# Kernel optimization log

Hardware: AMD Instinct MI355X
Metric: run time of the kernel (lower is better)

## Reference

```python
import jax, jax.numpy as jnp
import numpy as np

N, D, H1, K = 4096, 128, 256, 128


def setup_inputs() -> dict:
    key = jax.random.key(0)
    ks = jax.random.split(key, 8)
    A = jax.random.uniform(ks[3], (D, D), dtype=jnp.float32)
    A = A * (1.0 - jnp.eye(D, dtype=jnp.float32))  # DAG prob mask, no self-loops
    return {
        "x": jax.random.normal(ks[0], (N, D), dtype=jnp.float32),
        "weight": jax.random.normal(ks[1], (D, D), dtype=jnp.float32) * 0.1,
        "bias": jax.random.normal(ks[2], (1, D), dtype=jnp.float32) * 0.1,
        "A": A,
        "W1": jax.random.normal(ks[4], (D, H1), dtype=jnp.float32) * 0.1,
        "b1": jax.random.normal(ks[5], (H1,), dtype=jnp.float32) * 0.1,
        "W2": jax.random.normal(ks[6], (H1, K), dtype=jnp.float32) * 0.1,
        "b2": jax.random.normal(ks[7], (K,), dtype=jnp.float32) * 0.1,
    }


def reference(x, weight, bias, A, W1, b1, W2, b2):
    # to_adj (eval path): masked weights
    W = weight * A                                   # [D, D]
    y = x @ W + bias                                 # [N, D]
    # __expand__ builds diag(y[n]) [N,D,D]; since e[n,i,:] = y[n,i]*I[i,:],
    # the first Linear collapses to a per-row scaling of W1 (same math, fused):
    # e @ W1 -> y[n,i] * W1[i,:]
    h1 = jax.nn.relu(y[:, :, None] * W1[None, :, :] + b1)   # [N, D, H1]
    f = (h1 @ W2 + b2).sum(axis=2)                   # [N, D] (sum over output dim)
    # h_func, method='gnn'
    I = jnp.eye(D, dtype=x.dtype)
    A2 = jnp.square(W)
    M = I + A2 / D
    E = jnp.linalg.matrix_power(M, D - 1)
    h_val = (E.T * M).sum() - D
    # l1_reg (same prob mask in eval)
    reg = jnp.abs(W).sum()
    return (f, h_val, reg)
```

## Files before the change

kernel.cpp:

```cpp
#include <hip/hip_runtime.h>

#define NN 4096
#define DD 128
#define HH1 256

#define WS_S    0
#define WS_S2   16384
#define WS_S3   32768
#define WS_S4   49152
#define WS_W    65536
#define WS_W2S  81920
#define WS_PAIR 82176
#define WS_B2S  82688
#define WS_TACC 82696
#define WS_DONE 82708
#define WS_REGP 82712
#define WS_XT   82944
#define WS_REQ_FLOATS 607232
#define WS_REQ_BYTES  (WS_REQ_FLOATS * 4UL)

#define O_S    0
#define O_S2   16384
#define O_S3   32768
#define O_S4   49152
#define O_W2S  65536
#define O_B2S  65792
#define O_TACC 65808
#define O_DONE 65824
#define O_REGP 65840

__device__ __forceinline__ float waveReduce(float v) {
#pragma unroll
  for (int off = 32; off > 0; off >>= 1) v += __shfl_down(v, off, 64);
  return v;
}


__global__ __launch_bounds__(256) void kA2(
    const float* __restrict__ weight, const float* __restrict__ Amat,
    const float* __restrict__ W2, const float* __restrict__ b2,
    const float* __restrict__ b1v, const float* __restrict__ x,
    float* __restrict__ ws) {
  const int b = blockIdx.x, tid = threadIdx.x;
  __shared__ float s_lds[DD * DD];
  __shared__ float xs[128 * 133];
  if (b < 64) {
    const float4* w4 = (const float4*)weight;
    const float4* a4 = (const float4*)Amat;
    float4* s4 = (float4*)s_lds;
    const float inv = 1.0f / 128.0f;
    for (int e = tid; e < DD * DD / 4; e += 256) {
      float4 wv = w4[e], av = a4[e], o;
      float t;
      t = wv.x * av.x; o.x = t * t * inv;
      t = wv.y * av.y; o.y = t * t * inv;
      t = wv.z * av.z; o.z = t * t * inv;
      t = wv.w * av.w; o.w = t * t * inv;
      s4[e] = o;
    }
    __syncthreads();
    const int i = (b << 1) + (tid >> 7), j = tid & 127;
    const float* row = &s_lds[i * DD];
    float acc = 0.f;
#pragma unroll 8
    for (int k = 0; k < DD; ++k) acc = fmaf(row[k], s_lds[k * DD + j], acc);
    ws[WS_S2 + i * DD + j] = acc;
  } else if (b < 72) {
    const int base = (b - 64) * 2048;
    const float inv = 1.0f / 128.0f;
    for (int e = tid; e < 2048; e += 256) {
      const int idx = base + e;
      const float w = weight[idx] * Amat[idx];
      ws[WS_W + idx] = w;
      ws[WS_S + idx] = w * w * inv;
    }
  } else if (b == 72) {
    const float4* r = (const float4*)(W2 + tid * 128);
    float4 s4 = make_float4(0.f, 0.f, 0.f, 0.f);
#pragma unroll 8
    for (int k = 0; k < 32; ++k) {
      const float4 v = r[k];
      s4.x += v.x; s4.y += v.y; s4.z += v.z; s4.w += v.w;
    }
    const float w2sv = (s4.x + s4.y) + (s4.z + s4.w);
    ws[WS_W2S + tid] = w2sv;
    ((float2*)(ws + WS_PAIR))[tid] = make_float2(b1v[tid], w2sv);
  } else if (b == 73) {
    __shared__ float red[4];
    float v = (tid < 128) ? b2[tid] : 0.f;
    v = waveReduce(v);
    if ((tid & 63) == 0) red[tid >> 6] = v;
    __syncthreads();
    if (tid == 0) ws[WS_B2S] = (red[0] + red[1]) + (red[2] + red[3]);
    if (tid >= 64 && tid < 74) ws[WS_TACC + (tid - 64)] = 0.f;
    if (tid == 96) *(unsigned int*)(ws + WS_DONE) = 0u;
  } else if (b < 82) {
    const int bb = b - 74;
    const int base = bb * 2048;
    float s = 0.f;
    for (int e = tid; e < 2048; e += 256) {
      const int idx = base + e;
      s += fabsf(weight[idx] * Amat[idx]);
    }
    s = waveReduce(s);
    __shared__ float red2[4];
    if ((tid & 63) == 0) red2[tid >> 6] = s;
    __syncthreads();
    if (tid == 0) ws[WS_REGP + bb] = (red2[0] + red2[1]) + (red2[2] + red2[3]);
  } else {
    const int n0 = (b - 82) * 128;
    const float4* x4 = (const float4*)x;
    for (int e = tid; e < 4096; e += 256) {
      const int r = e >> 5, c = e & 31;
      const float4 v = x4[(n0 + r) * 32 + c];
      float* p = &xs[r * 133 + (c << 2)];
      p[0] = v.x; p[1] = v.y; p[2] = v.z; p[3] = v.w;
    }
    __syncthreads();
    float* xT = ws + WS_XT;
    const int c = tid & 31, ks = tid >> 5;
#pragma unroll 4
    for (int m = 0; m < 16; ++m) {
      const int k = ks + (m << 3);
      float4 o;
      o.x = xs[((c << 2) + 0) * 133 + k];
      o.y = xs[((c << 2) + 1) * 133 + k];
      o.z = xs[((c << 2) + 2) * 133 + k];
      o.w = xs[((c << 2) + 3) * 133 + k];
      *(float4*)&xT[k * NN + n0 + (c << 2)] = o;
    }
  }
}

__global__ __launch_bounds__(256) void kS34(float* __restrict__ ws) {
  const int tid = threadIdx.x;
  const int sb = blockIdx.x;
  const bool isS4 = sb >= 64;
  const int mb = isS4 ? sb - 64 : sb;
  const float* __restrict__ L = ws + WS_S2;
  const float* __restrict__ R = ws + (isS4 ? WS_S2 : WS_S);
  float* __restrict__ O = ws + (isS4 ? WS_S4 : WS_S3);
  const int i = (mb << 1) + (tid >> 7), j = tid & 127;
  float acc = 0.f;
#pragma unroll 8
  for (int k = 0; k < DD; ++k) acc = fmaf(L[i * DD + k], R[k * DD + j], acc);
  O[i * DD + j] = acc;
}

__global__ __launch_bounds__(256) void kC4(const float* __restrict__ W1,
                                           const float* __restrict__ bias,
                                           float* __restrict__ ws,
                                           float* __restrict__ out) {
  const int tid = threadIdx.x;
  if (blockIdx.x < 512) {
    __shared__ float ts[256 * 5];
    const int fb = blockIdx.x;
    const int n0 = (fb >> 5) << 8, i0 = (fb & 31) << 2;
    const int w = tid >> 6, l = tid & 63;
    const int iu = __builtin_amdgcn_readfirstlane(i0 + w);
    const float* __restrict__ xT = ws + WS_XT;
    const float* __restrict__ Wm = ws + WS_W;

    float t[4] = {0.f, 0.f, 0.f, 0.f};
#pragma unroll 8
    for (int k = 0; k < DD; ++k) {
      const float wv = Wm[k * DD + iu];
      const float4 xv = *(const float4*)&xT[k * NN + n0 + (l << 2)];
      t[0] = fmaf(xv.x, wv, t[0]);
      t[1] = fmaf(xv.y, wv, t[1]);
      t[2] = fmaf(xv.z, wv, t[2]);
      t[3] = fmaf(xv.w, wv, t[3]);
    }
    const float bv = bias[iu];
#pragma unroll
    for (int q = 0; q < 4; ++q) t[q] += bv;

    const float sb2 = ws[WS_B2S];
    float acc[4];
#pragma unroll
    for (int q = 0; q < 4; ++q) acc[q] = sb2;
    const float* __restrict__ W1row = W1 + iu * HH1;
    const float2* __restrict__ pr = (const float2*)(ws + WS_PAIR);
#pragma unroll 8
    for (int j = 0; j < HH1; ++j) {
      const float sw1 = W1row[j];
      const float2 p = pr[j];
      const float vb = p.x;
#pragma unroll
      for (int q = 0; q < 4; ++q) {
        const float h = fmaxf(fmaf(t[q], sw1, vb), 0.f);
        acc[q] = fmaf(h, p.y, acc[q]);
      }
    }
#pragma unroll
    for (int q = 0; q < 4; ++q) ts[((l << 2) + q) * 5 + w] = acc[q];
    __syncthreads();
    const int m = tid;
    float4 o;
    o.x = ts[m * 5 + 0]; o.y = ts[m * 5 + 1];
    o.z = ts[m * 5 + 2]; o.w = ts[m * 5 + 3];
    *(float4*)&out[(n0 + m) * DD + i0] = o;
    return;
  }
  const int tb = blockIdx.x - 512;
  const int i = (tb << 1) + (tid >> 7), j = tid & 127;
  const float* S1 = ws + WS_S;
  const float* S2 = ws + WS_S2;
  const float* S3 = ws + WS_S3;
  const float* S4 = ws + WS_S4;
  const float a1 = S1[i * DD + j], a2 = S2[i * DD + j], a3 = S3[i * DD + j];
  const float b1t = S1[j * DD + i], b2t = S2[j * DD + i],
              b3t = S3[j * DD + i], b4t = S4[j * DD + i];
  float e7 = 0.f;
#pragma unroll 8
  for (int k = 0; k < DD; ++k) e7 = fmaf(S3[i * DD + k], S4[k * DD + j], e7);
  float c[10];
  c[0] = a1 * b1t; c[1] = a2 * b1t; c[2] = a2 * b2t; c[3] = a3 * b2t;
  c[4] = a3 * b3t; c[5] = a3 * b4t; c[6] = e7 * b1t; c[7] = e7 * b2t;
  c[8] = e7 * b3t; c[9] = e7 * b4t;
  __shared__ float red[4][10];
#pragma unroll
  for (int m = 0; m < 10; ++m) {
    const float v = waveReduce(c[m]);
    if ((tid & 63) == 0) red[tid >> 6][m] = v;
  }
  __syncthreads();
  if (tid == 0) {
    float* tacc = ws + WS_TACC;
    for (int m = 0; m < 10; ++m)
      atomicAdd(&tacc[m], (red[0][m] + red[1][m]) + (red[2][m] + red[3][m]));
    __threadfence();
    unsigned int* done = (unsigned int*)(ws + WS_DONE);
    const unsigned int old = atomicAdd(done, 1u);
    if (old == 63u) {
      __threadfence();
      double h = 0.0, C = 8128.0;
      for (int kk = 2; kk <= 11; ++kk) {
        const float tv = atomicAdd(&tacc[kk - 2], 0.0f);
        h += C * (double)tv;
        C = C * (double)(128 - kk) / (double)(kk + 1);
      }
      float reg = 0.f;
      for (int m = 0; m < 8; ++m) reg += ws[WS_REGP + m];
      out[NN * DD] = (float)h;
      out[NN * DD + 1] = reg;
    }
  }
}

__global__ __launch_bounds__(256) void kA_old(
    const float* __restrict__ weight, const float* __restrict__ Amat,
    const float* __restrict__ W2, const float* __restrict__ b2,
    float* __restrict__ ws) {
  const int b = blockIdx.x, tid = threadIdx.x;
  if (b < 64) {
    __shared__ float s_lds[DD * DD];
    const float4* w4 = (const float4*)weight;
    const float4* a4 = (const float4*)Amat;
    float4* s4 = (float4*)s_lds;
    const float inv = 1.0f / 128.0f;
    for (int e = tid; e < DD * DD / 4; e += 256) {
      float4 wv = w4[e], av = a4[e], o;
      float t;
      t = wv.x * av.x; o.x = t * t * inv;
      t = wv.y * av.y; o.y = t * t * inv;
      t = wv.z * av.z; o.z = t * t * inv;
      t = wv.w * av.w; o.w = t * t * inv;
      s4[e] = o;
    }
    __syncthreads();
    const int i = (b << 1) + (tid >> 7), j = tid & 127;
    const float* row = &s_lds[i * DD];
    float acc = 0.f;
#pragma unroll 8
    for (int k = 0; k < DD; ++k) acc = fmaf(row[k], s_lds[k * DD + j], acc);
    ws[O_S2 + i * DD + j] = acc;
  } else if (b < 72) {
    const int base = (b - 64) * 2048;
    const float inv = 1.0f / 128.0f;
    for (int e = tid; e < 2048; e += 256) {
      const int idx = base + e;
      const float w = weight[idx] * Amat[idx];
      ws[O_S + idx] = w * w * inv;
    }
  } else if (b == 72) {
    const float4* r = (const float4*)(W2 + tid * 128);
    float4 s4 = make_float4(0.f, 0.f, 0.f, 0.f);
#pragma unroll 8
    for (int k = 0; k < 32; ++k) {
      const float4 v = r[k];
      s4.x += v.x; s4.y += v.y; s4.z += v.z; s4.w += v.w;
    }
    ws[O_W2S + tid] = (s4.x + s4.y) + (s4.z + s4.w);
  } else if (b == 73) {
    __shared__ float red[4];
    float v = (tid < 128) ? b2[tid] : 0.f;
    v = waveReduce(v);
    if ((tid & 63) == 0) red[tid >> 6] = v;
    __syncthreads();
    if (tid == 0) ws[O_B2S] = (red[0] + red[1]) + (red[2] + red[3]);
    if (tid >= 64 && tid < 74) ws[O_TACC + (tid - 64)] = 0.f;
    if (tid == 96) *(unsigned int*)(ws + O_DONE) = 0u;
  } else {
    const int bb = b - 74;
    const int base = bb * 2048;
    float s = 0.f;
    for (int e = tid; e < 2048; e += 256) {
      const int idx = base + e;
      s += fabsf(weight[idx] * Amat[idx]);
    }
    s = waveReduce(s);
    __shared__ float red[4];
    if ((tid & 63) == 0) red[tid >> 6] = s;
    __syncthreads();
    if (tid == 0) ws[O_REGP + bb] = (red[0] + red[1]) + (red[2] + red[3]);
  }
}

__global__ __launch_bounds__(256) void kB_old(
    const float* __restrict__ x, const float* __restrict__ weight,
    const float* __restrict__ Amat, const float* __restrict__ bias,
    const float* __restrict__ W1, const float* __restrict__ b1v,
    float* __restrict__ ws, float* __restrict__ out) {
  const int tid = threadIdx.x;
  if (blockIdx.x < 128) {
    const int sb = blockIdx.x;
    const bool isS4 = sb >= 64;
    const int mb = isS4 ? sb - 64 : sb;
    const float* __restrict__ L = ws + O_S2;
    const float* __restrict__ R = ws + (isS4 ? O_S2 : O_S);
    float* __restrict__ O = ws + (isS4 ? O_S4 : O_S3);
    const int i = (mb << 1) + (tid >> 7), j = tid & 127;
    float acc = 0.f;
#pragma unroll 8
    for (int k = 0; k < DD; ++k) acc = fmaf(L[i * DD + k], R[k * DD + j], acc);
    O[i * DD + j] = acc;
    return;
  }
  __shared__ float xs[64 * 132];
  __shared__ float4 fq[4 * 256];
  __shared__ float wcol[4 * 128];
  __shared__ float ts[64 * 5];
  const int fb = blockIdx.x - 128;
  const int i0 = (fb & 31) << 2, n0 = (fb >> 5) << 6;
  const float4* x4 = (const float4*)x;
  for (int e = tid; e < 64 * 32; e += 256) {
    const int r = e >> 5, c = e & 31;
    *(float4*)&xs[r * 132 + (c << 2)] = x4[(n0 + r) * 32 + c];
  }
  for (int e = tid; e < 512; e += 256) {
    const int w = e >> 7, k = e & 127;
    const int gi = k * DD + i0 + w;
    wcol[(w << 7) + k] = weight[gi] * Amat[gi];
  }
  const float* w2s = ws + O_W2S;
  for (int e = tid; e < 1024; e += 256) {
    const int w = e >> 8, j = e & 255;
    fq[(w << 8) + j] = make_float4(W1[(i0 + w) * HH1 + j], b1v[j], w2s[j], 0.f);
  }
  __syncthreads();
  const int w = tid >> 6, l = tid & 63;
  float t = bias[i0 + w];
  const float4* xr = (const float4*)&xs[l * 132];
  const float4* wc = (const float4*)&wcol[w << 7];
#pragma unroll
  for (int k = 0; k < 32; ++k) {
    const float4 xv = xr[k], wv = wc[k];
    t = fmaf(xv.x, wv.x, t);
    t = fmaf(xv.y, wv.y, t);
    t = fmaf(xv.z, wv.z, t);
    t = fmaf(xv.w, wv.w, t);
  }
  float acc = ws[O_B2S];
  const float4* fp = &fq[w << 8];
#pragma unroll 8
  for (int j = 0; j < HH1; ++j) {
    const float4 c = fp[j];
    acc = fmaf(fmaxf(fmaf(t, c.x, c.y), 0.f), c.z, acc);
  }
  ts[l * 5 + w] = acc;
  __syncthreads();
  if (tid < 64) {
    const float4 o = make_float4(ts[tid * 5 + 0], ts[tid * 5 + 1],
                                 ts[tid * 5 + 2], ts[tid * 5 + 3]);
    *(float4*)&out[(n0 + tid) * DD + i0] = o;
  }
}

__global__ __launch_bounds__(256) void kC_old(float* __restrict__ ws,
                                              float* __restrict__ out) {
  const int tid = threadIdx.x;
  const int i = (blockIdx.x << 1) + (tid >> 7), j = tid & 127;
  const float* S1 = ws + O_S;
  const float* S2 = ws + O_S2;
  const float* S3 = ws + O_S3;
  const float* S4 = ws + O_S4;
  const float a1 = S1[i * DD + j], a2 = S2[i * DD + j], a3 = S3[i * DD + j];
  const float b1t = S1[j * DD + i], b2t = S2[j * DD + i],
              b3t = S3[j * DD + i], b4t = S4[j * DD + i];
  float e7 = 0.f;
#pragma unroll 8
  for (int k = 0; k < DD; ++k) e7 = fmaf(S3[i * DD + k], S4[k * DD + j], e7);
  float c[10];
  c[0] = a1 * b1t; c[1] = a2 * b1t; c[2] = a2 * b2t; c[3] = a3 * b2t;
  c[4] = a3 * b3t; c[5] = a3 * b4t; c[6] = e7 * b1t; c[7] = e7 * b2t;
  c[8] = e7 * b3t; c[9] = e7 * b4t;
  __shared__ float red[4][10];
#pragma unroll
  for (int m = 0; m < 10; ++m) {
    const float v = waveReduce(c[m]);
    if ((tid & 63) == 0) red[tid >> 6][m] = v;
  }
  __syncthreads();
  if (tid == 0) {
    float* tacc = ws + O_TACC;
    for (int m = 0; m < 10; ++m)
      atomicAdd(&tacc[m], (red[0][m] + red[1][m]) + (red[2][m] + red[3][m]));
    __threadfence();
    unsigned int* done = (unsigned int*)(ws + O_DONE);
    const unsigned int old = atomicAdd(done, 1u);
    if (old == 63u) {
      __threadfence();
      double h = 0.0, C = 8128.0;
      for (int kk = 2; kk <= 11; ++kk) {
        const float tv = atomicAdd(&tacc[kk - 2], 0.0f);
        h += C * (double)tv;
        C = C * (double)(128 - kk) / (double)(kk + 1);
      }
      float reg = 0.f;
      for (int m = 0; m < 8; ++m) reg += ws[O_REGP + m];
      out[NN * DD] = (float)h;
      out[NN * DD + 1] = reg;
    }
  }
}

extern "C" void kernel_launch(void* const* d_in, const int* in_sizes, int n_in,
                              void* d_out, int out_size, void* d_ws,
                              size_t ws_size, hipStream_t stream) {
  const float* x      = (const float*)d_in[0];
  const float* weight = (const float*)d_in[1];
  const float* bias   = (const float*)d_in[2];
  const float* Amat   = (const float*)d_in[3];
  const float* W1     = (const float*)d_in[4];
  const float* b1v    = (const float*)d_in[5];
  const float* W2     = (const float*)d_in[6];
  const float* b2     = (const float*)d_in[7];
  float* out = (float*)d_out;
  float* ws  = (float*)d_ws;

  if (ws_size >= WS_REQ_BYTES) {
    kA2<<<114, 256, 0, stream>>>(weight, Amat, W2, b2, b1v, x, ws);
    kS34<<<128, 256, 0, stream>>>(ws);
    kC4<<<576, 256, 0, stream>>>(W1, bias, ws, out);
  } else {
    kA_old<<<82, 256, 0, stream>>>(weight, Amat, W2, b2, ws);
    kB_old<<<128 + 2048, 256, 0, stream>>>(x, weight, Amat, bias, W1, b1v, ws,
                                           out);
    kC_old<<<64, 256, 0, stream>>>(ws, out);
  }
}
```

Before: 125.8 us.

## Halve rows per thread in fused MLP kernel and add transposed masked weight

The main f-computation kernel now gives each thread 2 rows instead of 4, which doubles the block count to 1024. The x-transpose blocks are also halved in size, so kA2 launches more blocks. A transposed copy of the masked weight W is written so each wave reads its row of W contiguously instead of with a strided column access. The aim is more parallelism and better latency hiding on the ALU-bound 256-wide hidden loop. The cost is more per-block overhead, less reuse of W1 and pair loads per thread, and half the threads sitting idle during the output store.

```diff
diff --git a/kernel.cpp b/kernel.cpp
--- a/kernel.cpp
+++ b/kernel.cpp
@@ -15,8 +15,9 @@
 #define WS_TACC 82696
 #define WS_DONE 82708
 #define WS_REGP 82712
-#define WS_XT   82944
-#define WS_REQ_FLOATS 607232
+#define WS_WT   82944
+#define WS_XT   99328
+#define WS_REQ_FLOATS 623616
 #define WS_REQ_BYTES  (WS_REQ_FLOATS * 4UL)
 
 #define O_S    0
@@ -43,7 +44,7 @@
     float* __restrict__ ws) {
   const int b = blockIdx.x, tid = threadIdx.x;
   __shared__ float s_lds[DD * DD];
-  __shared__ float xs[128 * 133];
+  __shared__ float xs[64 * 133];
   if (b < 64) {
     const float4* w4 = (const float4*)weight;
     const float4* a4 = (const float4*)Amat;
@@ -71,7 +72,9 @@
     for (int e = tid; e < 2048; e += 256) {
       const int idx = base + e;
       const float w = weight[idx] * Amat[idx];
+      const int k = idx >> 7, i = idx & 127;
       ws[WS_W + idx] = w;
+      ws[WS_WT + i * DD + k] = w;
       ws[WS_S + idx] = w * w * inv;
     }
   } else if (b == 72) {
@@ -108,9 +111,9 @@
     __syncthreads();
     if (tid == 0) ws[WS_REGP + bb] = (red2[0] + red2[1]) + (red2[2] + red2[3]);
   } else {
-    const int n0 = (b - 82) * 128;
+    const int n0 = (b - 82) * 64;
     const float4* x4 = (const float4*)x;
-    for (int e = tid; e < 4096; e += 256) {
+    for (int e = tid; e < 2048; e += 256) {
       const int r = e >> 5, c = e & 31;
       const float4 v = x4[(n0 + r) * 32 + c];
       float* p = &xs[r * 133 + (c << 2)];
@@ -118,10 +121,10 @@
     }
     __syncthreads();
     float* xT = ws + WS_XT;
-    const int c = tid & 31, ks = tid >> 5;
-#pragma unroll 4
-    for (int m = 0; m < 16; ++m) {
-      const int k = ks + (m << 3);
+    const int c = tid & 15, ks = tid >> 4;
+#pragma unroll
+    for (int m = 0; m < 8; ++m) {
+      const int k = ks + (m << 4);
       float4 o;
       o.x = xs[((c << 2) + 0) * 133 + k];
       o.y = xs[((c << 2) + 1) * 133 + k];
@@ -147,62 +150,58 @@
   O[i * DD + j] = acc;
 }
 
-__global__ __launch_bounds__(256) void kC4(const float* __restrict__ W1,
+__global__ __launch_bounds__(256) void kC5(const float* __restrict__ W1,
                                            const float* __restrict__ bias,
                                            float* __restrict__ ws,
                                            float* __restrict__ out) {
   const int tid = threadIdx.x;
-  if (blockIdx.x < 512) {
-    __shared__ float ts[256 * 5];
+  if (blockIdx.x < 1024) {
+    __shared__ float ts[128 * 5];
     const int fb = blockIdx.x;
-    const int n0 = (fb >> 5) << 8, i0 = (fb & 31) << 2;
+    const int n0 = (fb >> 5) << 7, i0 = (fb & 31) << 2;
     const int w = tid >> 6, l = tid & 63;
     const int iu = __builtin_amdgcn_readfirstlane(i0 + w);
     const float* __restrict__ xT = ws + WS_XT;
-    const float* __restrict__ Wm = ws + WS_W;
-
-    float t[4] = {0.f, 0.f, 0.f, 0.f};
+    const float* __restrict__ wr = ws + WS_WT + iu * DD;
+
+    float t0 = 0.f, t1 = 0.f;
 #pragma unroll 8
     for (int k = 0; k < DD; ++k) {
-      const float wv = Wm[k * DD + iu];
-      const float4 xv = *(const float4*)&xT[k * NN + n0 + (l << 2)];
-      t[0] = fmaf(xv.x, wv, t[0]);
-      t[1] = fmaf(xv.y, wv, t[1]);
-      t[2] = fmaf(xv.z, wv, t[2]);
-      t[3] = fmaf(xv.w, wv, t[3]);
+      const float wv = wr[k];
+      const float2 xv = *(const float2*)&xT[k * NN + n0 + (l << 1)];
+      t0 = fmaf(xv.x, wv, t0);
+      t1 = fmaf(xv.y, wv, t1);
     }
     const float bv = bias[iu];
-#pragma unroll
-    for (int q = 0; q < 4; ++q) t[q] += bv;
+    t0 += bv;
+    t1 += bv;
 
     const float sb2 = ws[WS_B2S];
-    float acc[4];
-#pragma unroll
-    for (int q = 0; q < 4; ++q) acc[q] = sb2;
+    float a0 = sb2, a1 = sb2;
     const float* __restrict__ W1row = W1 + iu * HH1;
     const float2* __restrict__ pr = (const float2*)(ws + WS_PAIR);
 #pragma unroll 8
     for (int j = 0; j < HH1; ++j) {
       const float sw1 = W1row[j];
       const float2 p = pr[j];
-      const float vb = p.x;
-#pragma unroll
-      for (int q = 0; q < 4; ++q) {
-        const float h = fmaxf(fmaf(t[q], sw1, vb), 0.f);
-        acc[q] = fmaf(h, p.y, acc[q]);
-      }
-    }
-#pragma unroll
-    for (int q = 0; q < 4; ++q) ts[((l << 2) + q) * 5 + w] = acc[q];
-    __syncthreads();
-    const int m = tid;
-    float4 o;
-    o.x = ts[m * 5 + 0]; o.y = ts[m * 5 + 1];
-    o.z = ts[m * 5 + 2]; o.w = ts[m * 5 + 3];
-    *(float4*)&out[(n0 + m) * DD + i0] = o;
+      const float h0 = fmaxf(fmaf(t0, sw1, p.x), 0.f);
+      const float h1 = fmaxf(fmaf(t1, sw1, p.x), 0.f);
+      a0 = fmaf(h0, p.y, a0);
+      a1 = fmaf(h1, p.y, a1);
+    }
+    ts[((l << 1) + 0) * 5 + w] = a0;
+    ts[((l << 1) + 1) * 5 + w] = a1;
+    __syncthreads();
+    if (tid < 128) {
+      const int m = tid;
+      float4 o;
+      o.x = ts[m * 5 + 0]; o.y = ts[m * 5 + 1];
+      o.z = ts[m * 5 + 2]; o.w = ts[m * 5 + 3];
+      *(float4*)&out[(n0 + m) * DD + i0] = o;
+    }
     return;
   }
-  const int tb = blockIdx.x - 512;
+  const int tb = blockIdx.x - 1024;
   const int i = (tb << 1) + (tid >> 7), j = tid & 127;
   const float* S1 = ws + WS_S;
   const float* S2 = ws + WS_S2;
@@ -450,9 +449,9 @@
   float* ws  = (float*)d_ws;
 
   if (ws_size >= WS_REQ_BYTES) {
-    kA2<<<114, 256, 0, stream>>>(weight, Amat, W2, b2, b1v, x, ws);
+    kA2<<<146, 256, 0, stream>>>(weight, Amat, W2, b2, b1v, x, ws);
     kS34<<<128, 256, 0, stream>>>(ws);
-    kC4<<<576, 256, 0, stream>>>(W1, bias, ws, out);
+    kC5<<<1088, 256, 0, stream>>>(W1, bias, ws, out);
   } else {
     kA_old<<<82, 256, 0, stream>>>(weight, Amat, W2, b2, ws);
     kB_old<<<128 + 2048, 256, 0, stream>>>(x, weight, Amat, bias, W1, b1v, ws,
```

Measured after the change: 125.5 us. Within noise of the previous version (-0.3%).

## Replace per-row ReLU MLP loop with piecewise-linear breakpoint lookup

Applied to the files above, without the earlier changes.

For each input dimension i, the sum over H1 of relu(y*W1[i,j]+b1[j])*w2s[j] is a piecewise-linear function of y. A new kernel precomputes its sorted breakpoints and prefix-summed slope and intercept tables, using a bitonic sort and a scan. The main kernel then evaluates f with an 8-step binary search in LDS and one FMA, replacing the 256-iteration loop. It also stores a transposed masked weight so the y computation reads contiguously, and splits the x transpose into smaller blocks. The costs are an extra precompute pass, more workspace, and possible float reassociation differences.

```diff
diff --git a/kernel.cpp b/kernel.cpp
--- a/kernel.cpp
+++ b/kernel.cpp
@@ -15,8 +15,12 @@
 #define WS_TACC 82696
 #define WS_DONE 82708
 #define WS_REGP 82712
-#define WS_XT   82944
-#define WS_REQ_FLOATS 607232
+#define WS_WT   82944
+#define WS_XT   99328
+#define WS_TH   623616
+#define WS_A    656384
+#define WS_B    689280
+#define WS_REQ_FLOATS 722176
 #define WS_REQ_BYTES  (WS_REQ_FLOATS * 4UL)
 
 #define O_S    0
@@ -43,7 +47,7 @@
     float* __restrict__ ws) {
   const int b = blockIdx.x, tid = threadIdx.x;
   __shared__ float s_lds[DD * DD];
-  __shared__ float xs[128 * 133];
+  __shared__ float xs[64 * 133];
   if (b < 64) {
     const float4* w4 = (const float4*)weight;
     const float4* a4 = (const float4*)Amat;
@@ -71,7 +75,9 @@
     for (int e = tid; e < 2048; e += 256) {
       const int idx = base + e;
       const float w = weight[idx] * Amat[idx];
+      const int k = idx >> 7, i = idx & 127;
       ws[WS_W + idx] = w;
+      ws[WS_WT + i * DD + k] = w;
       ws[WS_S + idx] = w * w * inv;
     }
   } else if (b == 72) {
@@ -108,9 +114,9 @@
     __syncthreads();
     if (tid == 0) ws[WS_REGP + bb] = (red2[0] + red2[1]) + (red2[2] + red2[3]);
   } else {
-    const int n0 = (b - 82) * 128;
+    const int n0 = (b - 82) * 64;
     const float4* x4 = (const float4*)x;
-    for (int e = tid; e < 4096; e += 256) {
+    for (int e = tid; e < 2048; e += 256) {
       const int r = e >> 5, c = e & 31;
       const float4 v = x4[(n0 + r) * 32 + c];
       float* p = &xs[r * 133 + (c << 2)];
@@ -118,10 +124,10 @@
     }
     __syncthreads();
     float* xT = ws + WS_XT;
-    const int c = tid & 31, ks = tid >> 5;
-#pragma unroll 4
-    for (int m = 0; m < 16; ++m) {
-      const int k = ks + (m << 3);
+    const int c = tid & 15, ks = tid >> 4;
+#pragma unroll
+    for (int m = 0; m < 8; ++m) {
+      const int k = ks + (m << 4);
       float4 o;
       o.x = xs[((c << 2) + 0) * 133 + k];
       o.y = xs[((c << 2) + 1) * 133 + k];
@@ -132,39 +138,120 @@
   }
 }
 
-__global__ __launch_bounds__(256) void kS34(float* __restrict__ ws) {
+__global__ __launch_bounds__(256) void kPS(const float* __restrict__ W1,
+                                           const float* __restrict__ b1v,
+                                           float* __restrict__ ws) {
   const int tid = threadIdx.x;
-  const int sb = blockIdx.x;
-  const bool isS4 = sb >= 64;
-  const int mb = isS4 ? sb - 64 : sb;
-  const float* __restrict__ L = ws + WS_S2;
-  const float* __restrict__ R = ws + (isS4 ? WS_S2 : WS_S);
-  float* __restrict__ O = ws + (isS4 ? WS_S4 : WS_S3);
-  const int i = (mb << 1) + (tid >> 7), j = tid & 127;
-  float acc = 0.f;
-#pragma unroll 8
-  for (int k = 0; k < DD; ++k) acc = fmaf(L[i * DD + k], R[k * DD + j], acc);
-  O[i * DD + j] = acc;
-}
-
-__global__ __launch_bounds__(256) void kC4(const float* __restrict__ W1,
-                                           const float* __restrict__ bias,
+  if (blockIdx.x < 128) {
+    const int sb = blockIdx.x;
+    const bool isS4 = sb >= 64;
+    const int mb = isS4 ? sb - 64 : sb;
+    const float* __restrict__ L = ws + WS_S2;
+    const float* __restrict__ R = ws + (isS4 ? WS_S2 : WS_S);
+    float* __restrict__ O = ws + (isS4 ? WS_S4 : WS_S3);
+    const int i = (mb << 1) + (tid >> 7), j = tid & 127;
+    float acc = 0.f;
+#pragma unroll 8
+    for (int k = 0; k < DD; ++k) acc = fmaf(L[i * DD + k], R[k * DD + j], acc);
+    O[i * DD + j] = acc;
+    return;
+  }
+  const int i = blockIdx.x - 128;
+  __shared__ float kT[256], kS[256], kC[256];
+  __shared__ float redb[8];
+  __shared__ float base2[2];
+  const int j = tid;
+  const float w = W1[i * HH1 + j];
+  const float w2s = ws[WS_W2S + j];
+  const float bj = b1v[j];
+  const float s = w * w2s, c = bj * w2s;
+  float th, ds, dc, bs, bc;
+  if (w > 0.f) {
+    th = -bj / w; ds = s; dc = c; bs = 0.f; bc = 0.f;
+  } else if (w < 0.f) {
+    th = -bj / w; ds = -s; dc = -c; bs = s; bc = c;
+  } else {
+    th = 3.4e38f; ds = 0.f; dc = 0.f; bs = 0.f; bc = fmaxf(bj, 0.f) * w2s;
+  }
+  {
+    const float rs = waveReduce(bs), rc = waveReduce(bc);
+    if ((tid & 63) == 0) {
+      redb[tid >> 6] = rs;
+      redb[4 + (tid >> 6)] = rc;
+    }
+  }
+  kT[tid] = th; kS[tid] = ds; kC[tid] = dc;
+  __syncthreads();
+  if (tid == 0) {
+    base2[0] = (redb[0] + redb[1]) + (redb[2] + redb[3]);
+    base2[1] = (redb[4] + redb[5]) + (redb[6] + redb[7]);
+  }
+  for (int kk = 2; kk <= 256; kk <<= 1) {
+    for (int jj = kk >> 1; jj > 0; jj >>= 1) {
+      __syncthreads();
+      const int ixj = tid ^ jj;
+      if (ixj > tid) {
+        const bool up = ((tid & kk) == 0);
+        const float ta = kT[tid], tb = kT[ixj];
+        if ((ta > tb) == up) {
+          kT[tid] = tb; kT[ixj] = ta;
+          const float sa = kS[tid], sb = kS[ixj];
+          kS[tid] = sb; kS[ixj] = sa;
+          const float ca = kC[tid], cb = kC[ixj];
+          kC[tid] = cb; kC[ixj] = ca;
+        }
+      }
+    }
+  }
+  __syncthreads();
+  for (int off = 1; off < 256; off <<= 1) {
+    float vs = 0.f, vc = 0.f;
+    if (tid >= off) { vs = kS[tid - off]; vc = kC[tid - off]; }
+    __syncthreads();
+    kS[tid] += vs; kC[tid] += vc;
+    __syncthreads();
+  }
+  const float b_s = base2[0], b_c = base2[1];
+  ws[WS_TH + i * 256 + tid] = kT[tid];
+  ws[WS_A + i * 257 + tid + 1] = b_s + kS[tid];
+  ws[WS_B + i * 257 + tid + 1] = b_c + kC[tid];
+  if (tid == 0) {
+    ws[WS_A + i * 257] = b_s;
+    ws[WS_B + i * 257] = b_c;
+  }
+}
+
+__global__ __launch_bounds__(256) void kC6(const float* __restrict__ bias,
                                            float* __restrict__ ws,
                                            float* __restrict__ out) {
   const int tid = threadIdx.x;
   if (blockIdx.x < 512) {
+    __shared__ float lT[4 * 256];
+    __shared__ float lA[4 * 257];
+    __shared__ float lB[4 * 257];
     __shared__ float ts[256 * 5];
     const int fb = blockIdx.x;
     const int n0 = (fb >> 5) << 8, i0 = (fb & 31) << 2;
     const int w = tid >> 6, l = tid & 63;
     const int iu = __builtin_amdgcn_readfirstlane(i0 + w);
+
+#pragma unroll
+    for (int q = 0; q < 4; ++q) {
+      lT[(q << 8) + tid] = ws[WS_TH + (i0 + q) * 256 + tid];
+      lA[q * 257 + tid] = ws[WS_A + (i0 + q) * 257 + tid];
+      lB[q * 257 + tid] = ws[WS_B + (i0 + q) * 257 + tid];
+      if (tid == 0) {
+        lA[q * 257 + 256] = ws[WS_A + (i0 + q) * 257 + 256];
+        lB[q * 257 + 256] = ws[WS_B + (i0 + q) * 257 + 256];
+      }
+    }
+
     const float* __restrict__ xT = ws + WS_XT;
-    const float* __restrict__ Wm = ws + WS_W;
-
+    const float* __restrict__ wr = ws + WS_WT + iu * DD;
     float t[4] = {0.f, 0.f, 0.f, 0.f};
 #pragma unroll 8
     for (int k = 0; k < DD; ++k) {
-      const float wv = Wm[k * DD + iu];
+      const float wv = wr[k];
       const float4 xv = *(const float4*)&xT[k * NN + n0 + (l << 2)];
       t[0] = fmaf(xv.x, wv, t[0]);
       t[1] = fmaf(xv.y, wv, t[1]);
@@ -172,28 +259,23 @@
       t[3] = fmaf(xv.w, wv, t[3]);
     }
     const float bv = bias[iu];
-#pragma unroll
-    for (int q = 0; q < 4; ++q) t[q] += bv;
-
     const float sb2 = ws[WS_B2S];
-    float acc[4];
-#pragma unroll
-    for (int q = 0; q < 4; ++q) acc[q] = sb2;
-    const float* __restrict__ W1row = W1 + iu * HH1;
-    const float2* __restrict__ pr = (const float2*)(ws + WS_PAIR);
-#pragma unroll 8
-    for (int j = 0; j < HH1; ++j) {
-      const float sw1 = W1row[j];
-      const float2 p = pr[j];
-      const float vb = p.x;
-#pragma unroll
-      for (int q = 0; q < 4; ++q) {
-        const float h = fmaxf(fmaf(t[q], sw1, vb), 0.f);
-        acc[q] = fmaf(h, p.y, acc[q]);
+    __syncthreads();
+
+    const float* Tw = &lT[w << 8];
+    const float* Aw = &lA[w * 257];
+    const float* Bw = &lB[w * 257];
+#pragma unroll
+    for (int q = 0; q < 4; ++q) {
+      const float yq = t[q] + bv;
+      int m = 0;
+#pragma unroll
+      for (int st = 128; st > 0; st >>= 1) {
+        if (Tw[m + st - 1] <= yq) m += st;
       }
-    }
-#pragma unroll
-    for (int q = 0; q < 4; ++q) ts[((l << 2) + q) * 5 + w] = acc[q];
+      const float f = fmaf(Aw[m], yq, Bw[m]) + sb2;
+      ts[((l << 2) + q) * 5 + w] = f;
+    }
     __syncthreads();
     const int m = tid;
     float4 o;
@@ -450,9 +532,9 @@
   float* ws  = (float*)d_ws;
 
   if (ws_size >= WS_REQ_BYTES) {
-    kA2<<<114, 256, 0, stream>>>(weight, Amat, W2, b2, b1v, x, ws);
-    kS34<<<128, 256, 0, stream>>>(ws);
-    kC4<<<576, 256, 0, stream>>>(W1, bias, ws, out);
+    kA2<<<146, 256, 0, stream>>>(weight, Amat, W2, b2, b1v, x, ws);
+    kPS<<<256, 256, 0, stream>>>(W1, b1v, ws);
+    kC6<<<576, 256, 0, stream>>>(bias, ws, out);
   } else {
     kA_old<<<82, 256, 0, stream>>>(weight, Amat, W2, b2, ws);
     kB_old<<<128 + 2048, 256, 0, stream>>>(x, weight, Amat, bias, W1, b1v, ws,
```

New measurement: 116.5 us. 7.4% less time.
